# Optimization experiments

Measured on AMD Instinct MI355X. Metric: run time of the kernel, lower is better.

The kernel has to match this reference:

```python
import jax, jax.numpy as jnp
import numpy as np

B, T, I, H = 65536, 9, 57, 2  # batch, seq_len, input_size, hidden_size


def setup_inputs() -> dict:
    key = jax.random.key(0)
    ks = jax.random.split(key, 7)
    return {
        "x": jax.random.normal(ks[0], (B, T, I), dtype=jnp.float32),
        "W_ih": jax.random.normal(ks[1], (4 * H, I), dtype=jnp.float32) * 0.1,
        "W_hh": jax.random.normal(ks[2], (4 * H, H), dtype=jnp.float32) * 0.1,
        "b_ih": jax.random.normal(ks[3], (4 * H,), dtype=jnp.float32) * 0.1,
        "b_hh": jax.random.normal(ks[4], (4 * H,), dtype=jnp.float32) * 0.1,
        "fc_w": jax.random.normal(ks[5], (1, H), dtype=jnp.float32) * 0.1,
        "fc_b": jax.random.normal(ks[6], (1,), dtype=jnp.float32) * 0.1,
    }


def reference(x, W_ih, W_hh, b_ih, b_hh, fc_w, fc_b):
    # Precompute input contribution to the gates for all timesteps: [B, T, 4H]
    gx = jnp.einsum("bti,gi->btg", x, W_ih) + b_ih + b_hh
    h0 = jnp.zeros((x.shape[0], W_hh.shape[1]), dtype=x.dtype)
    c0 = jnp.zeros_like(h0)

    def step(carry, g_t):
        h, c = carry
        g = g_t + h @ W_hh.T  # [B, 4H]
        i, f, gg, o = jnp.split(g, 4, axis=-1)  # PyTorch gate order: i, f, g, o
        i = jax.nn.sigmoid(i)
        f = jax.nn.sigmoid(f)
        gg = jnp.tanh(gg)
        o = jax.nn.sigmoid(o)
        c = f * c + i * gg
        h = o * jnp.tanh(c)
        return (h, c), None

    (h_T, _), _ = jax.lax.scan(step, (h0, c0), jnp.swapaxes(gx, 0, 1))  # scan over time
    # fc applied to last hidden state: [B, 1]
    return h_T @ fc_w.T + fc_b
```

## Files before the change

kernel.cpp:

```cpp
#include <hip/hip_runtime.h>


#define B_TOTAL 65536
#define T_STEPS 9
#define I_DIM   57
#define BATCH_PER_BLOCK 64
#define ROWS_PER_BLOCK (BATCH_PER_BLOCK * T_STEPS)
#define CHUNK_ROWS 64
#define N_CHUNKS   (ROWS_PER_BLOCK / CHUNK_ROWS)
#define CHUNK_DW   (CHUNK_ROWS * I_DIM)
#define CHUNK_F4   (CHUNK_DW / 4)
#define GX_PAD     9
#define NBLOCKS    (B_TOTAL / BATCH_PER_BLOCK)

__device__ __forceinline__ float fast_tanh(float v) {
    float e = __builtin_amdgcn_exp2f(2.885390082f * v);
    return 1.0f - 2.0f * __builtin_amdgcn_rcpf(e + 1.0f);
}
__device__ __forceinline__ float fast_sig(float v) {
    return 0.5f * fast_tanh(0.5f * v) + 0.5f;
}

#define DPP_ROR_F32(VAR, SRC, CTRL)                                          \
    float VAR = __builtin_bit_cast(float, __builtin_amdgcn_update_dpp(       \
        0, __builtin_bit_cast(int, SRC), (CTRL), 0xF, 0xF, false))

__device__ __forceinline__ void gload_lds16(const float* g, float* l) {
    __builtin_amdgcn_global_load_lds(
        (const __attribute__((address_space(1))) void*)g,
        (__attribute__((address_space(3))) void*)l,
        16, 0, 0);
}

__global__ __launch_bounds__(256)
void lstm_onepass(const float* __restrict__ x,
                  const float* __restrict__ W_ih,
                  const float* __restrict__ W_hh,
                  const float* __restrict__ b_ih,
                  const float* __restrict__ b_hh,
                  const float* __restrict__ fc_w,
                  const float* __restrict__ fc_b,
                  float* __restrict__ out) {
    __shared__ float xs[2][CHUNK_DW];
    __shared__ float gxp[ROWS_PER_BLOCK * GX_PAD];

    const int tid  = threadIdx.x;
    const int wv   = tid >> 6;
    const int lane = tid & 63;
    const int cl   = (lane >> 4) & 3;
    const int g    = (lane >> 1) & 7;
    const int p    = lane & 1;

    float wrot[8][8];
#pragma unroll
    for (int d = 0; d < 8; ++d) {
        const int gg = (g + d) & 7;
        const float* wr = W_ih + gg * I_DIM;
#pragma unroll
        for (int k = 0; k < 7; ++k) wrot[d][k] = wr[g + 8 * k];
        wrot[d][7] = (g == 0) ? wr[56] : 0.0f;
    }
    float bsum = b_ih[g] + b_hh[g];
#pragma unroll
    for (int d = 0; d < 8; ++d)
#pragma unroll
        for (int k = 0; k < 8; ++k)
            asm volatile("" : "+v"(wrot[d][k]));

    const float* xblk = x + (size_t)blockIdx.x * (ROWS_PER_BLOCK * I_DIM);

#define GLOAD(C, S) do {                                                    \
        const float* gc_ = xblk + (size_t)(C) * CHUNK_DW;                   \
        float* lb_ = &xs[S][0] + wv * 256;          \
        gload_lds16(gc_ + tid * 4,        lb_);                             \
        gload_lds16(gc_ + (256 + tid) * 4, lb_ + 1024);                     \
        gload_lds16(gc_ + (512 + tid) * 4, lb_ + 2048);                     \
        if (tid < CHUNK_F4 - 768)                                           \
            gload_lds16(gc_ + (768 + tid) * 4, lb_ + 3072);                 \
    } while (0)

#define COMPUTE(S, C) do {                                                  \
        _Pragma("unroll")                                                   \
        for (int iter = 0; iter < 2; ++iter) {                              \
            const int rl_ = wv * 16 + iter * 8 + cl * 2 + p;                \
            const float* row_ = xs[S] + rl_ * I_DIM;                        \
            float xv_[8];                                                   \
            _Pragma("unroll")                                               \
            for (int k = 0; k < 7; ++k) xv_[k] = row_[g + 8 * k];           \
            xv_[7] = row_[56];        \
            float acc_[8];                                                  \
            _Pragma("unroll")                                               \
            for (int d = 0; d < 8; ++d) {                                   \
                float s_ = wrot[d][0] * xv_[0];                             \
                _Pragma("unroll")                                           \
                for (int k = 1; k < 8; ++k) s_ += wrot[d][k] * xv_[k];      \
                acc_[d] = s_;                                               \
            }                                                               \
                       \
            DPP_ROR_F32(r1_, acc_[1], 0x122);                               \
            DPP_ROR_F32(r2_, acc_[2], 0x124);                               \
            DPP_ROR_F32(r3_, acc_[3], 0x126);                               \
            DPP_ROR_F32(r4_, acc_[4], 0x128);                               \
            DPP_ROR_F32(r5_, acc_[5], 0x12A);                               \
            DPP_ROR_F32(r6_, acc_[6], 0x12C);                               \
            DPP_ROR_F32(r7_, acc_[7], 0x12E);                               \
            float tot_ = ((acc_[0] + r1_) + (r2_ + r3_))                    \
                       + ((r4_ + r5_) + (r6_ + r7_)) + bsum;                \
            gxp[((C) * CHUNK_ROWS + rl_) * GX_PAD + g] = tot_;              \
        }                                                                   \
    } while (0)

    GLOAD(0, 0);
    __syncthreads();

#pragma unroll
    for (int cc = 0; cc < N_CHUNKS; ++cc) {
        if (cc + 1 < N_CHUNKS) GLOAD(cc + 1, (cc + 1) & 1);
        COMPUTE(cc & 1, cc);
        __syncthreads();
    }
#undef GLOAD
#undef COMPUTE

    if (tid < BATCH_PER_BLOCK) {
        float w0[8], w1[8];
#pragma unroll
        for (int q = 0; q < 8; ++q) {
            w0[q] = W_hh[q * 2];
            w1[q] = W_hh[q * 2 + 1];
        }

        float h0 = 0.f, h1 = 0.f, c0 = 0.f, c1 = 0.f;
        const float* gb = gxp + tid * (T_STEPS * GX_PAD);

#pragma unroll
        for (int t = 0; t < T_STEPS; ++t) {
            const float* pp = gb + t * GX_PAD;
            const float i0 = fast_sig (pp[0] + h0 * w0[0] + h1 * w1[0]);
            const float i1 = fast_sig (pp[1] + h0 * w0[1] + h1 * w1[1]);
            const float f0 = fast_sig (pp[2] + h0 * w0[2] + h1 * w1[2]);
            const float f1 = fast_sig (pp[3] + h0 * w0[3] + h1 * w1[3]);
            const float g0 = fast_tanh(pp[4] + h0 * w0[4] + h1 * w1[4]);
            const float g1 = fast_tanh(pp[5] + h0 * w0[5] + h1 * w1[5]);
            const float o0 = fast_sig (pp[6] + h0 * w0[6] + h1 * w1[6]);
            const float o1 = fast_sig (pp[7] + h0 * w0[7] + h1 * w1[7]);
            c0 = f0 * c0 + i0 * g0;
            c1 = f1 * c1 + i1 * g1;
            h0 = o0 * fast_tanh(c0);
            h1 = o1 * fast_tanh(c1);
        }

        out[blockIdx.x * BATCH_PER_BLOCK + tid] =
            h0 * fc_w[0] + h1 * fc_w[1] + fc_b[0];
    }
}

extern "C" void kernel_launch(void* const* d_in, const int* in_sizes, int n_in,
                              void* d_out, int out_size, void* d_ws, size_t ws_size,
                              hipStream_t stream) {
    const float* x    = (const float*)d_in[0];
    const float* W_ih = (const float*)d_in[1];
    const float* W_hh = (const float*)d_in[2];
    const float* b_ih = (const float*)d_in[3];
    const float* b_hh = (const float*)d_in[4];
    const float* fc_w = (const float*)d_in[5];
    const float* fc_b = (const float*)d_in[6];
    float* out = (float*)d_out;

    lstm_onepass<<<dim3(NBLOCKS), dim3(256), 0, stream>>>(
        x, W_ih, W_hh, b_ih, b_hh, fc_w, fc_b, out);
}
```

Baseline: 39.02 us.

## Make each wave process its own rows with register-staged loads and no barriers

Each wave now owns a contiguous 144-row slice (16 batch elements × 9 steps). It loads that slice in 16-row chunks into registers, double-buffered in two float4 register sets, and writes them to a wave-private LDS buffer. This replaces the block-wide global_load_lds double buffer and removes every __syncthreads. The x[56] term is now added per lane after the DPP reduction instead of through a zero-padded weight column. The recurrence is split so 16 lanes per wave handle their own batch elements, and launch bounds now request 4 blocks per CU. The aim is to cut barrier stalls and let waves progress independently. The cost is more vector registers and an extra register-to-LDS copy.

```diff
diff --git a/kernel.cpp b/kernel.cpp
--- a/kernel.cpp
+++ b/kernel.cpp
@@ -6,12 +6,13 @@
 #define I_DIM   57
 #define BATCH_PER_BLOCK 64
 #define ROWS_PER_BLOCK (BATCH_PER_BLOCK * T_STEPS)
-#define CHUNK_ROWS 64
-#define N_CHUNKS   (ROWS_PER_BLOCK / CHUNK_ROWS)
-#define CHUNK_DW   (CHUNK_ROWS * I_DIM)
-#define CHUNK_F4   (CHUNK_DW / 4)
-#define GX_PAD     9
-#define NBLOCKS    (B_TOTAL / BATCH_PER_BLOCK)
+#define ROWS_PER_WAVE  144
+#define WCH_ROWS 16
+#define N_WCH    9
+#define WCH_DW   (WCH_ROWS * I_DIM)
+#define WCH_F4   (WCH_DW / 4)
+#define GX_PAD   9
+#define NBLOCKS  (B_TOTAL / BATCH_PER_BLOCK)
 
 __device__ __forceinline__ float fast_tanh(float v) {
     float e = __builtin_amdgcn_exp2f(2.885390082f * v);
@@ -25,14 +26,7 @@
     float VAR = __builtin_bit_cast(float, __builtin_amdgcn_update_dpp(       \
         0, __builtin_bit_cast(int, SRC), (CTRL), 0xF, 0xF, false))
 
-__device__ __forceinline__ void gload_lds16(const float* g, float* l) {
-    __builtin_amdgcn_global_load_lds(
-        (const __attribute__((address_space(1))) void*)g,
-        (__attribute__((address_space(3))) void*)l,
-        16, 0, 0);
-}
-
-__global__ __launch_bounds__(256)
+__global__ __launch_bounds__(256, 4)
 void lstm_onepass(const float* __restrict__ x,
                   const float* __restrict__ W_ih,
                   const float* __restrict__ W_hh,
@@ -41,9 +35,8 @@
                   const float* __restrict__ fc_w,
                   const float* __restrict__ fc_b,
                   float* __restrict__ out) {
-    __shared__ float xs[2][CHUNK_DW];
+    __shared__ float xs[4][WCH_DW];
     __shared__ float gxp[ROWS_PER_BLOCK * GX_PAD];
-
     const int tid  = threadIdx.x;
     const int wv   = tid >> 6;
     const int lane = tid & 63;
@@ -51,49 +44,60 @@
     const int g    = (lane >> 1) & 7;
     const int p    = lane & 1;
 
-    float wrot[8][8];
+    float wrot[8][7];
 #pragma unroll
     for (int d = 0; d < 8; ++d) {
         const int gg = (g + d) & 7;
         const float* wr = W_ih + gg * I_DIM;
 #pragma unroll
         for (int k = 0; k < 7; ++k) wrot[d][k] = wr[g + 8 * k];
-        wrot[d][7] = (g == 0) ? wr[56] : 0.0f;
     }
+    float w56  = W_ih[g * I_DIM + 56];
     float bsum = b_ih[g] + b_hh[g];
 #pragma unroll
     for (int d = 0; d < 8; ++d)
 #pragma unroll
-        for (int k = 0; k < 8; ++k)
+        for (int k = 0; k < 7; ++k)
             asm volatile("" : "+v"(wrot[d][k]));
+    asm volatile("" : "+v"(w56), "+v"(bsum));
 
-    const float* xblk = x + (size_t)blockIdx.x * (ROWS_PER_BLOCK * I_DIM);
+    const float* xw = x + (size_t)blockIdx.x * (ROWS_PER_BLOCK * I_DIM)
+                        + (size_t)wv * (ROWS_PER_WAVE * I_DIM);
+    float* xsw = xs[wv];
 
-#define GLOAD(C, S) do {                                                    \
-        const float* gc_ = xblk + (size_t)(C) * CHUNK_DW;                   \
-        float* lb_ = &xs[S][0] + wv * 256;          \
-        gload_lds16(gc_ + tid * 4,        lb_);                             \
-        gload_lds16(gc_ + (256 + tid) * 4, lb_ + 1024);                     \
-        gload_lds16(gc_ + (512 + tid) * 4, lb_ + 2048);                     \
-        if (tid < CHUNK_F4 - 768)                                           \
-            gload_lds16(gc_ + (768 + tid) * 4, lb_ + 3072);                 \
+    float4 a0, a1, a2, a3, b0, b1, b2, b3;
+
+#define SLOAD(C, R0, R1, R2, R3) do {                                       \
+        const float4* xc_ = (const float4*)(xw + (size_t)(C) * WCH_DW);     \
+        R0 = xc_[lane];                                                     \
+        R1 = xc_[64 + lane];                                                \
+        R2 = xc_[128 + lane];                                               \
+        if (lane < WCH_F4 - 192) R3 = xc_[192 + lane];                      \
     } while (0)
 
-#define COMPUTE(S, C) do {                                                  \
+#define SWRITE(R0, R1, R2, R3) do {                                         \
+        float4* L_ = (float4*)xsw;                                          \
+        L_[lane] = R0;                                                      \
+        L_[64 + lane] = R1;                                                 \
+        L_[128 + lane] = R2;                                                \
+        if (lane < WCH_F4 - 192) L_[192 + lane] = R3;                       \
+    } while (0)
+
+#define COMPUTE(C) do {                                                     \
         _Pragma("unroll")                                                   \
         for (int iter = 0; iter < 2; ++iter) {                              \
-            const int rl_ = wv * 16 + iter * 8 + cl * 2 + p;                \
-            const float* row_ = xs[S] + rl_ * I_DIM;                        \
-            float xv_[8];                                                   \
+            const int rin_ = iter * 8 + cl * 2 + p;                         \
+            const float* row_ = xsw + rin_ * I_DIM;                         \
+            float xv_[7];                                                   \
             _Pragma("unroll")                                               \
             for (int k = 0; k < 7; ++k) xv_[k] = row_[g + 8 * k];           \
-            xv_[7] = row_[56];        \
+            const float x56_ = row_[56];                                    \
             float acc_[8];                                                  \
             _Pragma("unroll")                                               \
             for (int d = 0; d < 8; ++d) {                                   \
                 float s_ = wrot[d][0] * xv_[0];                             \
                 _Pragma("unroll")                                           \
-                for (int k = 1; k < 8; ++k) s_ += wrot[d][k] * xv_[k];      \
+                for (int k = 1; k < 7; ++k) s_ += wrot[d][k] * xv_[k];      \
                 acc_[d] = s_;                                               \
             }                                                               \
                        \
@@ -105,24 +109,33 @@
             DPP_ROR_F32(r6_, acc_[6], 0x12C);                               \
             DPP_ROR_F32(r7_, acc_[7], 0x12E);                               \
             float tot_ = ((acc_[0] + r1_) + (r2_ + r3_))                    \
-                       + ((r4_ + r5_) + (r6_ + r7_)) + bsum;                \
-            gxp[((C) * CHUNK_ROWS + rl_) * GX_PAD + g] = tot_;              \
+                       + ((r4_ + r5_) + (r6_ + r7_))                        \
+                       + bsum + w56 * x56_;                                 \
+            gxp[(wv * ROWS_PER_WAVE + (C) * WCH_ROWS + rin_) * GX_PAD + g]  \
+                = tot_;                                                     \
         }                                                                   \
     } while (0)
 
-    GLOAD(0, 0);
-    __syncthreads();
+    SLOAD(0, a0, a1, a2, a3);
+    SWRITE(a0, a1, a2, a3);
+    SLOAD(1, b0, b1, b2, b3);
 
 #pragma unroll
-    for (int cc = 0; cc < N_CHUNKS; ++cc) {
-        if (cc + 1 < N_CHUNKS) GLOAD(cc + 1, (cc + 1) & 1);
-        COMPUTE(cc & 1, cc);
-        __syncthreads();
+    for (int cc = 0; cc < N_WCH; ++cc) {
+        COMPUTE(cc);
+        if ((cc & 1) == 0) {
+            if (cc + 2 < N_WCH) SLOAD(cc + 2, a0, a1, a2, a3);
+            if (cc + 1 < N_WCH) SWRITE(b0, b1, b2, b3);
+        } else {
+            if (cc + 2 < N_WCH) SLOAD(cc + 2, b0, b1, b2, b3);
+            if (cc + 1 < N_WCH) SWRITE(a0, a1, a2, a3);
+        }
     }
-#undef GLOAD
+#undef SLOAD
+#undef SWRITE
 #undef COMPUTE
 
-    if (tid < BATCH_PER_BLOCK) {
+    if (lane < 16) {
         float w0[8], w1[8];
 #pragma unroll
         for (int q = 0; q < 8; ++q) {
@@ -130,9 +143,9 @@
             w1[q] = W_hh[q * 2 + 1];
         }
 
+        const int bloc = wv * 16 + lane;
         float h0 = 0.f, h1 = 0.f, c0 = 0.f, c1 = 0.f;
-        const float* gb = gxp + tid * (T_STEPS * GX_PAD);
-
+        const float* gb = gxp + bloc * (T_STEPS * GX_PAD);
 #pragma unroll
         for (int t = 0; t < T_STEPS; ++t) {
             const float* pp = gb + t * GX_PAD;
@@ -150,7 +163,7 @@
             h1 = o1 * fast_tanh(c1);
         }
 
-        out[blockIdx.x * BATCH_PER_BLOCK + tid] =
+        out[blockIdx.x * BATCH_PER_BLOCK + bloc] =
             h0 * fc_w[0] + h1 * fc_w[1] + fc_b[0];
     }
 }
```

After: 34.20 us. 1.14x faster.
